# Performance work log

Measured on AMD Instinct MI355X. Metric: run time of the kernel, lower is better.

Reference implementation:

```python
import jax, jax.numpy as jnp
import numpy as np

SIGMA = 1.0
TEMPERATURE = 1.0
GAMMA = 1.0 / (2.0 * SIGMA ** 2)


def setup_inputs() -> dict:
    key = jax.random.key(0)
    k1, k2 = jax.random.split(key)
    B, N, D = 8, 1024, 128
    features_nc = jax.random.normal(k1, (B, N, D), dtype=jnp.float32)
    features_c = jax.random.normal(k2, (B, N, D), dtype=jnp.float32)
    return {"features_nc": features_nc, "features_c": features_c}


def reference(features_nc, features_c):
    D = features_nc.shape[-1]
    x = features_nc.reshape(-1, D)   # (K, D)
    y = features_c.reshape(-1, D)    # (K, D)
    K = x.shape[0]
    x_sq = jnp.sum(x * x, axis=1, keepdims=True)          # (K, 1)
    y_sq = jnp.sum(y * y, axis=1, keepdims=True)          # (K, 1)
    sq_dist = x_sq + y_sq.T - 2.0 * jnp.matmul(x, y.T)    # (K, K)
    logits = (-GAMMA / TEMPERATURE) * sq_dist
    # cross-entropy with labels = arange(K): mean over rows of -log_softmax diag
    log_probs = jax.nn.log_softmax(logits, axis=-1)
    diag = jnp.diagonal(log_probs)
    loss = -jnp.mean(diag)
    return loss
```

## Files before the change

### kernel.cpp

```cpp
#include <hip/hip_runtime.h>
#include <hip/hip_bf16.h>
#include <math.h>

#define KROWS 8192
#define DDIM  128
#define RT    128
#define CTILE 128
#define NTILES 64
#define NRB   64
#define NC0   12
#define TILEB (CTILE * DDIM * 2)
#define SHIFT 94.0f

static constexpr float LOG2E_F = 1.44269504088896340736f;
static constexpr float LN2_F   = 0.69314718055994530942f;

typedef __attribute__((ext_vector_type(8))) short short8;
typedef __attribute__((ext_vector_type(4))) float float4v;

#if __has_builtin(__builtin_amdgcn_exp2f)
#define EXP2(x) __builtin_amdgcn_exp2f(x)
#else
#define EXP2(x) exp2f(x)
#endif

#define AS1C(p) ((const __attribute__((address_space(1))) void*)(p))
#define AS3(p)  ((__attribute__((address_space(3))) void*)(p))

static __device__ __forceinline__ unsigned short f2bf(float f) {
    __hip_bfloat16 h = __float2bfloat16(f);
    return *reinterpret_cast<unsigned short*>(&h);
}

__global__ __launch_bounds__(256) void prep_kernel(
    const float* __restrict__ x, const float* __restrict__ y,
    unsigned int* __restrict__ xb, unsigned int* __restrict__ yb,
    float* __restrict__ xsq2, float* __restrict__ ysq2,
    float* __restrict__ diagn, float* __restrict__ pl)
{
    const int w = threadIdx.x >> 6, lane = threadIdx.x & 63;
    const int row = blockIdx.x * 4 + w;
    if (blockIdx.x < KROWS / 256) pl[blockIdx.x * 256 + threadIdx.x] = 0.0f;
    const float2 xv = *reinterpret_cast<const float2*>(x + (size_t)row * DDIM + lane * 2);
    const float2 yv = *reinterpret_cast<const float2*>(y + (size_t)row * DDIM + lane * 2);
    xb[(size_t)row * 64 + lane] = (unsigned int)f2bf(xv.x * LOG2E_F)
                                | ((unsigned int)f2bf(xv.y * LOG2E_F) << 16);
    yb[(size_t)row * 64 + lane] = (unsigned int)f2bf(yv.x) | ((unsigned int)f2bf(yv.y) << 16);
    float xx = xv.x * xv.x + xv.y * xv.y;
    float yy = yv.x * yv.x + yv.y * yv.y;
    float xy = xv.x * yv.x + xv.y * yv.y;
    #pragma unroll
    for (int o = 32; o > 0; o >>= 1) {
        xx += __shfl_xor(xx, o, 64);
        yy += __shfl_xor(yy, o, 64);
        xy += __shfl_xor(xy, o, 64);
    }
    if (lane == 0) {
        xsq2[row] = fmaf(-0.5f * xx, LOG2E_F, SHIFT);
        ysq2[row] = -0.5f * yy * LOG2E_F;
        diagn[row] = xy - 0.5f * (xx + yy);
    }
}

__global__ __launch_bounds__(256, 2) void gemm_lse_kernel(
    const unsigned short* __restrict__ xb, const unsigned short* __restrict__ yb,
    const float* __restrict__ xsq2, const float* __restrict__ ysq2,
    float* __restrict__ pl)
{
    __shared__ alignas(16) unsigned char Ys[TILEB];

    const int t = threadIdx.x;
    const int w = t >> 6, lane = t & 63, quad = lane >> 4, lo = lane & 15;
    const int rb = (blockIdx.x & (NRB - 1)) * RT;
    const int c0 = blockIdx.x >> 6;

    short8 af[2][4];
    #pragma unroll
    for (int ri = 0; ri < 2; ri++)
        #pragma unroll
        for (int kk = 0; kk < 4; kk++)
            af[ri][kk] = *reinterpret_cast<const short8*>(
                xb + (size_t)(rb + w * 32 + ri * 16 + lo) * DDIM + kk * 32 + quad * 8);

    float a2v[8];
    #pragma unroll
    for (int ri = 0; ri < 2; ri++)
        #pragma unroll
        for (int r = 0; r < 4; r++)
            a2v[ri * 4 + r] = xsq2[rb + w * 32 + ri * 16 + quad * 4 + r];

    float sums[8];
    #pragma unroll
    for (int i = 0; i < 8; i++) sums[i] = 0.0f;

    const int gswz = ((t >> 4) << 8) + (((t & 15) ^ ((t >> 4) & 7)) << 4);
    int base_k[4];
    #pragma unroll
    for (int kk = 0; kk < 4; kk++)
        base_k[kk] = lo * 256 + ((((kk << 2) + quad) ^ (lo & 7)) << 4);

    {
        const char* g = (const char*)yb + (size_t)c0 * TILEB + gswz;
        #pragma unroll
        for (int q = 0; q < 8; q++)
            __builtin_amdgcn_global_load_lds(AS1C(g + q * 4096),
                                             AS3(&Ys[(q * 256 + t) * 16]), 16, 0, 0);
    }
    __syncthreads();

    int ct = c0;
    while (true) {
        float b2[8];
        #pragma unroll
        for (int ci = 0; ci < 8; ci++) b2[ci] = ysq2[ct * CTILE + ci * 16 + lo];

        float4v acc[2][8];
        #pragma unroll
        for (int ri = 0; ri < 2; ri++)
            #pragma unroll
            for (int ci = 0; ci < 8; ci++)
                acc[ri][ci] = (float4v){a2v[ri * 4 + 0] + b2[ci], a2v[ri * 4 + 1] + b2[ci],
                                        a2v[ri * 4 + 2] + b2[ci], a2v[ri * 4 + 3] + b2[ci]};

        #pragma unroll
        for (int kk = 0; kk < 4; kk++) {
            #pragma unroll
            for (int ci = 0; ci < 8; ci++) {
                short8 b = *reinterpret_cast<const short8*>(&Ys[base_k[kk] + ci * 4096]);
                acc[0][ci] = __builtin_amdgcn_mfma_f32_16x16x32_bf16(af[0][kk], b, acc[0][ci], 0, 0, 0);
                acc[1][ci] = __builtin_amdgcn_mfma_f32_16x16x32_bf16(af[1][kk], b, acc[1][ci], 0, 0, 0);
            }
        }
        __syncthreads();

        const int ctn = ct + NC0;
        if (ctn < NTILES) {
            const char* g = (const char*)yb + (size_t)ctn * TILEB + gswz;
            #pragma unroll
            for (int q = 0; q < 8; q++)
                __builtin_amdgcn_global_load_lds(AS1C(g + q * 4096),
                                                 AS3(&Ys[(q * 256 + t) * 16]), 16, 0, 0);
        }

        #pragma unroll
        for (int ri = 0; ri < 2; ri++)
            #pragma unroll
            for (int r = 0; r < 4; r++) {
                float s = 0.0f;
                #pragma unroll
                for (int ci = 0; ci < 8; ci++)
                    s += EXP2(acc[ri][ci][r]);
                sums[ri * 4 + r] += s;
            }

        if (ctn >= NTILES) break;
        ct = ctn;
        __syncthreads();
    }

    #pragma unroll
    for (int i = 0; i < 8; i++) {
        float s = sums[i];
        s += __shfl_xor(s, 1, 64);
        s += __shfl_xor(s, 2, 64);
        s += __shfl_xor(s, 4, 64);
        s += __shfl_xor(s, 8, 64);
        if (lo == 0) {
            int row = rb + w * 32 + (i >> 2) * 16 + quad * 4 + (i & 3);
            atomicAdd(&pl[row], s);
        }
    }
}

__global__ __launch_bounds__(1024) void finish_kernel(
    const float* __restrict__ pl, const float* __restrict__ diagn,
    float* __restrict__ out)
{
    const int t = threadIdx.x;
    float acc = 0.0f;
    for (int r = t; r < KROWS; r += 1024)
        acc += (log2f(pl[r]) - SHIFT) * LN2_F - diagn[r];
    #pragma unroll
    for (int o = 32; o > 0; o >>= 1) acc += __shfl_down(acc, o, 64);
    __shared__ float ws[16];
    if ((t & 63) == 0) ws[t >> 6] = acc;
    __syncthreads();
    if (t == 0) {
        float s = 0.0f;
        #pragma unroll
        for (int i = 0; i < 16; i++) s += ws[i];
        out[0] = s * (1.0f / KROWS);
    }
}

extern "C" void kernel_launch(void* const* d_in, const int* in_sizes, int n_in,
                              void* d_out, int out_size, void* d_ws, size_t ws_size,
                              hipStream_t stream) {
    const float* x = (const float*)d_in[0];
    const float* y = (const float*)d_in[1];
    float* out = (float*)d_out;

    unsigned short* xb = (unsigned short*)d_ws;
    unsigned short* yb = xb + (size_t)KROWS * DDIM;
    float* xsq2  = (float*)(yb + (size_t)KROWS * DDIM);
    float* ysq2  = xsq2 + KROWS;
    float* diagn = ysq2 + KROWS;
    float* pl    = diagn + KROWS;

    prep_kernel<<<KROWS / 4, 256, 0, stream>>>(x, y, (unsigned int*)xb, (unsigned int*)yb,
                                               xsq2, ysq2, diagn, pl);
    gemm_lse_kernel<<<NRB * NC0, 256, 0, stream>>>(xb, yb, xsq2, ysq2, pl);
    finish_kernel<<<1, 1024, 0, stream>>>(pl, diagn, out);
}
```

Baseline: 87.28 us.

## Double-buffer smaller column tiles and raise occupancy in fused GEMM-LSE kernel

Halves the column tile to 64, adds a two-slot LDS buffer so the next tile's global-to-LDS load is issued before computing on the current one, and removes one barrier per iteration. Grid becomes 64x16 blocks, each with a fixed, fully unrolled 8-iteration loop instead of the uneven 12-way column split, and launch bounds ask for 4 blocks per CU. The aim is to hide load latency and balance work across CUs. In exchange, each MFMA batch is smaller, LDS-read reuse per tile drops, and the register budget per thread is tighter.

```diff
diff --git a/kernel.cpp b/kernel.cpp
--- a/kernel.cpp
+++ b/kernel.cpp
@@ -5,10 +5,10 @@
 #define KROWS 8192
 #define DDIM  128
 #define RT    128
-#define CTILE 128
-#define NTILES 64
-#define NRB   64
-#define NC0   12
+#define CTILE 64
+#define NTILES (KROWS / CTILE)
+#define NCB   16
+#define NITER (NTILES / NCB)
 #define TILEB (CTILE * DDIM * 2)
 #define SHIFT 94.0f
 
@@ -62,16 +62,16 @@
     }
 }
 
-__global__ __launch_bounds__(256, 2) void gemm_lse_kernel(
+__global__ __launch_bounds__(256, 4) void gemm_lse_kernel(
     const unsigned short* __restrict__ xb, const unsigned short* __restrict__ yb,
     const float* __restrict__ xsq2, const float* __restrict__ ysq2,
     float* __restrict__ pl)
 {
-    __shared__ alignas(16) unsigned char Ys[TILEB];
+    __shared__ alignas(16) unsigned char Ys[2][TILEB];
 
     const int t = threadIdx.x;
     const int w = t >> 6, lane = t & 63, quad = lane >> 4, lo = lane & 15;
-    const int rb = (blockIdx.x & (NRB - 1)) * RT;
+    const int rb = (blockIdx.x & 63) * RT;
     const int c0 = blockIdx.x >> 6;
 
     short8 af[2][4];
@@ -102,45 +102,45 @@
     {
         const char* g = (const char*)yb + (size_t)c0 * TILEB + gswz;
         #pragma unroll
-        for (int q = 0; q < 8; q++)
+        for (int q = 0; q < 4; q++)
             __builtin_amdgcn_global_load_lds(AS1C(g + q * 4096),
-                                             AS3(&Ys[(q * 256 + t) * 16]), 16, 0, 0);
+                                             AS3(&Ys[0][(q * 256 + t) * 16]), 16, 0, 0);
     }
     __syncthreads();
 
-    int ct = c0;
-    while (true) {
-        float b2[8];
-        #pragma unroll
-        for (int ci = 0; ci < 8; ci++) b2[ci] = ysq2[ct * CTILE + ci * 16 + lo];
-
-        float4v acc[2][8];
+    #pragma unroll
+    for (int k = 0; k < NITER; k++) {
+        const int ct = c0 + k * NCB;
+
+        if (k + 1 < NITER) {
+            const char* g = (const char*)yb + (size_t)(ct + NCB) * TILEB + gswz;
+            #pragma unroll
+            for (int q = 0; q < 4; q++)
+                __builtin_amdgcn_global_load_lds(AS1C(g + q * 4096),
+                                                 AS3(&Ys[(k + 1) & 1][(q * 256 + t) * 16]), 16, 0, 0);
+        }
+
+        float b2[4];
+        #pragma unroll
+        for (int ci = 0; ci < 4; ci++) b2[ci] = ysq2[ct * CTILE + ci * 16 + lo];
+
+        float4v acc[2][4];
         #pragma unroll
         for (int ri = 0; ri < 2; ri++)
             #pragma unroll
-            for (int ci = 0; ci < 8; ci++)
+            for (int ci = 0; ci < 4; ci++)
                 acc[ri][ci] = (float4v){a2v[ri * 4 + 0] + b2[ci], a2v[ri * 4 + 1] + b2[ci],
                                         a2v[ri * 4 + 2] + b2[ci], a2v[ri * 4 + 3] + b2[ci]};
 
         #pragma unroll
         for (int kk = 0; kk < 4; kk++) {
             #pragma unroll
-            for (int ci = 0; ci < 8; ci++) {
-                short8 b = *reinterpret_cast<const short8*>(&Ys[base_k[kk] + ci * 4096]);
+            for (int ci = 0; ci < 4; ci++) {
+                short8 b = *reinterpret_cast<const short8*>(&Ys[k & 1][base_k[kk] + ci * 4096]);
                 acc[0][ci] = __builtin_amdgcn_mfma_f32_16x16x32_bf16(af[0][kk], b, acc[0][ci], 0, 0, 0);
                 acc[1][ci] = __builtin_amdgcn_mfma_f32_16x16x32_bf16(af[1][kk], b, acc[1][ci], 0, 0, 0);
             }
         }
-        __syncthreads();
-
-        const int ctn = ct + NC0;
-        if (ctn < NTILES) {
-            const char* g = (const char*)yb + (size_t)ctn * TILEB + gswz;
-            #pragma unroll
-            for (int q = 0; q < 8; q++)
-                __builtin_amdgcn_global_load_lds(AS1C(g + q * 4096),
-                                                 AS3(&Ys[(q * 256 + t) * 16]), 16, 0, 0);
-        }
 
         #pragma unroll
         for (int ri = 0; ri < 2; ri++)
@@ -148,13 +148,11 @@
             for (int r = 0; r < 4; r++) {
                 float s = 0.0f;
                 #pragma unroll
-                for (int ci = 0; ci < 8; ci++)
+                for (int ci = 0; ci < 4; ci++)
                     s += EXP2(acc[ri][ci][r]);
                 sums[ri * 4 + r] += s;
             }
 
-        if (ctn >= NTILES) break;
-        ct = ctn;
         __syncthreads();
     }
 
@@ -209,6 +207,6 @@
 
     prep_kernel<<<KROWS / 4, 256, 0, stream>>>(x, y, (unsigned int*)xb, (unsigned int*)yb,
                                                xsq2, ysq2, diagn, pl);
-    gemm_lse_kernel<<<NRB * NC0, 256, 0, stream>>>(xb, yb, xsq2, ysq2, pl);
+    gemm_lse_kernel<<<64 * NCB, 256, 0, stream>>>(xb, yb, xsq2, ysq2, pl);
     finish_kernel<<<1, 1024, 0, stream>>>(pl, diagn, out);
 }
```

After: 194.9 us. 123% more time.
